# Kernel optimization log

Hardware: AMD Instinct MI355X
Metric: run time of the kernel (lower is better)

## Reference

```python
import jax, jax.numpy as jnp
import numpy as np


def _parallel_scan_affine(log_a, b):
    """Hillis-Steele doubling scan for h_t = a_t*h_{t-1} + b_t (h_0 = 0).

    log_a, b: (B, T, d). Operator: (la2,b2) o (la1,b1) = (la1+la2, exp(la2)*b1 + b2).
    """
    T = log_a.shape[1]
    la, bv = log_a, b
    stride = 1
    while stride < T:  # static Python loop, log2(T) rounds
        la_prev = jnp.roll(la, stride, axis=1).at[:, :stride, :].set(0.0)
        bv_prev = jnp.roll(bv, stride, axis=1).at[:, :stride, :].set(0.0)
        bv = jnp.exp(la) * bv_prev + bv
        la = la + la_prev
        stride *= 2
    return bv


def setup_inputs() -> dict:
    key = jax.random.key(0)
    kx, kwz, kwh = jax.random.split(key, 3)
    B, T, D = 4, 4096, 1024
    x = jax.random.normal(kx, (B, T, D), dtype=jnp.float32)
    # nn.Linear(D, D) weights, stored as (out, in) like torch
    Wz = jax.random.normal(kwz, (D, D), dtype=jnp.float32) * 0.02
    bz = jnp.zeros((D,), dtype=jnp.float32)
    Wh = jax.random.normal(kwh, (D, D), dtype=jnp.float32) * 0.02
    bh = jnp.zeros((D,), dtype=jnp.float32)
    return {"x": x, "Wz": Wz, "bz": bz, "Wh": Wh, "bh": bh}


def reference(x, Wz, bz, Wh, bh):
    # forward_parallel: z = sigmoid(linear_z(x)); h_tilde = linear_h(x)
    z = jax.nn.sigmoid(jnp.einsum("btd,ed->bte", x, Wz) + bz)
    h_tilde = jnp.einsum("btd,ed->bte", x, Wh) + bh
    log_a = jnp.log(1.0 - z + 1e-08)
    b = z * h_tilde
    h_out = _parallel_scan_affine(log_a, b)
    return h_out  # out_proj is Identity since d_inner == d_model
```

## Files before the change

kernel.cpp:

```cpp
#include <hip/hip_runtime.h>
#include <hip/hip_bf16.h>


typedef __bf16 bf16x8 __attribute__((ext_vector_type(8)));
typedef __bf16 bf16x4 __attribute__((ext_vector_type(4)));
typedef float  f32x4  __attribute__((ext_vector_type(4)));

#define BSZ 4
#define TSZ 4096
#define DSZ 1024
#define MSZ (BSZ*TSZ)
#define CH  32
#define NC  (TSZ/CH)

__device__ __forceinline__ void gload_lds16(const __bf16* g, __bf16* l) {
  __builtin_amdgcn_global_load_lds(
      (const __attribute__((address_space(1))) void*)g,
      (__attribute__((address_space(3))) void*)l, 16, 0, 0);
}

__global__ void convert_tile_kernel(const float* __restrict__ X,
                                    const float* __restrict__ Wz,
                                    const float* __restrict__ Wh,
                                    __bf16* __restrict__ Xc,
                                    __bf16* __restrict__ Wzc,
                                    __bf16* __restrict__ Whc)
{
  const int bx = blockIdx.x;
  const float* src; __bf16* dst; int gid;
  if (bx < 8192)      { src = X;  dst = Xc;  gid =  bx        *256 + threadIdx.x; }
  else if (bx < 8704) { src = Wz; dst = Wzc; gid = (bx - 8192)*256 + threadIdx.x; }
  else                { src = Wh; dst = Whc; gid = (bx - 8704)*256 + threadIdx.x; }
  const int l    = gid & 63;
  const int i    = (gid >> 6) & 7;
  const int kblk = (gid >> 9) & 31;
  const int rblk = gid >> 14;
  const int row  = rblk*128 + i*16 + (l & 15);
  const int col  = kblk*32 + (l >> 4)*8;
  const float* g = src + (size_t)row*DSZ + col;
  float4 v0 = *(const float4*)g;
  float4 v1 = *(const float4*)(g + 4);
  bf16x8 p;
  p[0]=(__bf16)v0.x; p[1]=(__bf16)v0.y; p[2]=(__bf16)v0.z; p[3]=(__bf16)v0.w;
  p[4]=(__bf16)v1.x; p[5]=(__bf16)v1.y; p[6]=(__bf16)v1.z; p[7]=(__bf16)v1.w;
  *(bf16x8*)(dst + (size_t)gid*8) = p;
}

__global__ __launch_bounds__(256, 2) void gemm_gate_kernel(
    const __bf16* __restrict__ Xc,  const __bf16* __restrict__ Wzc,
    const __bf16* __restrict__ Whc,
    const float* __restrict__ bz, const float* __restrict__ bh,
    __bf16* __restrict__ a_ws, float* __restrict__ b_out)
{
  __shared__ __align__(16) __bf16 As [4096];
  __shared__ __align__(16) __bf16 Bzs[4096];
  __shared__ __align__(16) __bf16 Bhs[4096];

  const int tid  = threadIdx.x;
  const int lane = tid & 63;
  const int wv   = tid >> 6;
  const int wM   = (wv >> 1) * 64;
  const int wN   = (wv & 1) * 64;
  const int wMg  = wM >> 4;
  const int wNg  = wN >> 4;
  const int lr   = lane & 15;
  const int q    = lane >> 4;
  const int wbase = wv * 64;

  const __bf16* Xb = Xc  + (size_t)blockIdx.x * 32 * 4096;
  const __bf16* Zb = Wzc + (size_t)blockIdx.y * 32 * 4096;
  const __bf16* Hb = Whc + (size_t)blockIdx.y * 32 * 4096;

  f32x4 accz[4][4] = {};
  f32x4 acch[4][4] = {};

  for (int kblk = 0; kblk < 32; ++kblk) {
    __syncthreads();
    const size_t tb = (size_t)kblk * 4096;
    #pragma unroll
    for (int c = 0; c < 2; ++c) {
      const int eo = (c*256 + wbase + lane) * 8;
      const int lo = (c*256 + wbase) * 8;
      gload_lds16(Xb + tb + eo, As  + lo);
      gload_lds16(Zb + tb + eo, Bzs + lo);
      gload_lds16(Hb + tb + eo, Bhs + lo);
    }
    __syncthreads();

    bf16x8 af[4];
    #pragma unroll
    for (int i = 0; i < 4; ++i)
      af[i] = *(const bf16x8*)(As + (wMg + i)*512 + lane*8);
    #pragma unroll
    for (int j = 0; j < 4; ++j) {
      bf16x8 bz8 = *(const bf16x8*)(Bzs + (wNg + j)*512 + lane*8);
      bf16x8 bh8 = *(const bf16x8*)(Bhs + (wNg + j)*512 + lane*8);
      #pragma unroll
      for (int i = 0; i < 4; ++i) {
        accz[j][i] = __builtin_amdgcn_mfma_f32_16x16x32_bf16(af[i], bz8, accz[j][i], 0, 0, 0);
        acch[j][i] = __builtin_amdgcn_mfma_f32_16x16x32_bf16(af[i], bh8, acch[j][i], 0, 0, 0);
      }
    }
  }

  const int M0 = blockIdx.x * 128;
  const int N0 = blockIdx.y * 128;
  #pragma unroll
  for (int j = 0; j < 4; ++j) {
    const int e = N0 + wN + j*16 + lr;
    const float bzv = bz[e];
    const float bhv = bh[e];
    #pragma unroll
    for (int i = 0; i < 4; ++i) {
      const int mbase = M0 + wM + i*16 + q*4;
      #pragma unroll
      for (int r = 0; r < 4; ++r) {
        const size_t idx = (size_t)(mbase + r)*DSZ + e;
        const float pz = accz[j][i][r] + bzv;
        const float ph = acch[j][i][r] + bhv;
        const float ex = __expf(-pz);
        const float z  = 1.0f / (1.0f + ex);
        a_ws[idx]  = (__bf16)fmaf(ex, z, 1e-8f);
        b_out[idx] = z * ph;
      }
    }
  }
}

__global__ void scan_pass1_kernel(const __bf16* __restrict__ a_ws,
                                  const float* __restrict__ b_out,
                                  float* __restrict__ Aprod,
                                  float* __restrict__ Bcomp)
{
  const int bc   = blockIdx.x;
  const int d0   = threadIdx.x * 4;
  const size_t base = (size_t)bc * CH * DSZ + d0;
  float A[4]  = {1.f, 1.f, 1.f, 1.f};
  float Bv[4] = {0.f, 0.f, 0.f, 0.f};
  #pragma unroll 8
  for (int t = 0; t < CH; ++t) {
    bf16x4 a4 = *(const bf16x4*)(a_ws + base + (size_t)t*DSZ);
    float4 b4 = *(const float4*)(b_out + base + (size_t)t*DSZ);
    const float bb[4] = {b4.x, b4.y, b4.z, b4.w};
    #pragma unroll
    for (int c = 0; c < 4; ++c) {
      const float a = (float)a4[c];
      Bv[c] = fmaf(a, Bv[c], bb[c]);
      A[c] *= a;
    }
  }
  const size_t cidx = (size_t)bc*DSZ + d0;
  *(float4*)(Aprod + cidx) = make_float4(A[0], A[1], A[2], A[3]);
  *(float4*)(Bcomp + cidx) = make_float4(Bv[0], Bv[1], Bv[2], Bv[3]);
}

__global__ void scan_pass2_kernel(const float* __restrict__ Aprod,
                                  const float* __restrict__ Bcomp,
                                  float* __restrict__ Hstart)
{
  const int lane = threadIdx.x & 63;
  const int wave = (blockIdx.x * 256 + threadIdx.x) >> 6;
  const int b = wave >> 10;
  const int d = wave & 1023;
  const size_t i0 = (size_t)(b*NC + 2*lane)*DSZ + d;
  const float A0 = Aprod[i0],       B0 = Bcomp[i0];
  const float A1 = Aprod[i0 + DSZ], B1 = Bcomp[i0 + DSZ];
  float A  = A0 * A1;
  float Bv = fmaf(A1, B0, B1);
  #pragma unroll
  for (int s = 1; s < 64; s <<= 1) {
    const float Ap = __shfl_up(A,  s, 64);
    const float Bp = __shfl_up(Bv, s, 64);
    if (lane >= s) { Bv = fmaf(A, Bp, Bv); A *= Ap; }
  }
  float Hp = __shfl_up(Bv, 1, 64);
  if (lane == 0) Hp = 0.0f;
  Hstart[i0]       = Hp;
  Hstart[i0 + DSZ] = fmaf(A0, Hp, B0);
}

__global__ void scan_pass3_kernel(const __bf16* __restrict__ a_ws,
                                  const float* __restrict__ Hstart,
                                  float* __restrict__ out)
{
  const int bc   = blockIdx.x;
  const int d0   = threadIdx.x * 4;
  const size_t base = (size_t)bc * CH * DSZ + d0;
  float4 hv = *(const float4*)(Hstart + (size_t)bc*DSZ + d0);
  float h[4] = {hv.x, hv.y, hv.z, hv.w};
  #pragma unroll 8
  for (int t = 0; t < CH; ++t) {
    bf16x4 a4 = *(const bf16x4*)(a_ws + base + (size_t)t*DSZ);
    float4 b4 = *(const float4*)(out + base + (size_t)t*DSZ);
    const float bb[4] = {b4.x, b4.y, b4.z, b4.w};
    #pragma unroll
    for (int c = 0; c < 4; ++c)
      h[c] = fmaf((float)a4[c], h[c], bb[c]);
    *(float4*)(out + base + (size_t)t*DSZ) = make_float4(h[0], h[1], h[2], h[3]);
  }
}

extern "C" void kernel_launch(void* const* d_in, const int* in_sizes, int n_in,
                              void* d_out, int out_size, void* d_ws, size_t ws_size,
                              hipStream_t stream)
{
  const float* x  = (const float*)d_in[0];
  const float* Wz = (const float*)d_in[1];
  const float* bz = (const float*)d_in[2];
  const float* Wh = (const float*)d_in[3];
  const float* bh = (const float*)d_in[4];
  float* out = (float*)d_out;

  __bf16* Xc   = (__bf16*)d_ws;
  __bf16* Wzc  = Xc  + (size_t)MSZ * DSZ;
  __bf16* Whc  = Wzc + (size_t)DSZ * DSZ;
  __bf16* a_ws = Whc + (size_t)DSZ * DSZ;
  float* Aprod  = (float*)(a_ws + (size_t)MSZ * DSZ);
  float* Bcomp  = Aprod + (size_t)BSZ*NC*DSZ;
  float* Hstart = Bcomp + (size_t)BSZ*NC*DSZ;

  convert_tile_kernel<<<9216, 256, 0, stream>>>(x, Wz, Wh, Xc, Wzc, Whc);
  gemm_gate_kernel<<<dim3(MSZ/128, DSZ/128), 256, 0, stream>>>(Xc, Wzc, Whc, bz, bh, a_ws, out);
  scan_pass1_kernel<<<BSZ*NC, 256, 0, stream>>>(a_ws, out, Aprod, Bcomp);
  scan_pass2_kernel<<<(BSZ*DSZ)/4, 256, 0, stream>>>(Aprod, Bcomp, Hstart);
  scan_pass3_kernel<<<BSZ*NC, 256, 0, stream>>>(a_ws, Hstart, out);
}
```

Baseline: 255.6 us.

## Fuse chunk-local scan reduction into GEMM epilogue, drop scan pass1 kernel

The GEMM epilogue now computes the per-32-row chunk affine composition (A product, B combination) directly from its accumulator values, using in-register sequential combine over 4 rows and cross-quad shuffles, and writes Aprod/Bcomp. This removes the separate scan_pass1 kernel and its full re-read of a_ws and b_out from global memory. In exchange it adds shuffles and register pressure to the GEMM epilogue, and relies on the MFMA output row mapping matching chunk boundaries.

```diff
diff --git a/kernel.cpp b/kernel.cpp
--- a/kernel.cpp
+++ b/kernel.cpp
@@ -50,7 +50,8 @@
     const __bf16* __restrict__ Xc,  const __bf16* __restrict__ Wzc,
     const __bf16* __restrict__ Whc,
     const float* __restrict__ bz, const float* __restrict__ bh,
-    __bf16* __restrict__ a_ws, float* __restrict__ b_out)
+    __bf16* __restrict__ a_ws, float* __restrict__ b_out,
+    float* __restrict__ Aprod, float* __restrict__ Bcomp)
 {
   __shared__ __align__(16) __bf16 As [4096];
   __shared__ __align__(16) __bf16 Bzs[4096];
@@ -110,9 +111,11 @@
     const int e = N0 + wN + j*16 + lr;
     const float bzv = bz[e];
     const float bhv = bh[e];
+    float Aseg[4], Bseg[4];
     #pragma unroll
     for (int i = 0; i < 4; ++i) {
       const int mbase = M0 + wM + i*16 + q*4;
+      float A = 1.0f, Bv = 0.0f;
       #pragma unroll
       for (int r = 0; r < 4; ++r) {
         const size_t idx = (size_t)(mbase + r)*DSZ + e;
@@ -120,38 +123,36 @@
         const float ph = acch[j][i][r] + bhv;
         const float ex = __expf(-pz);
         const float z  = 1.0f / (1.0f + ex);
-        a_ws[idx]  = (__bf16)fmaf(ex, z, 1e-8f);
-        b_out[idx] = z * ph;
-      }
-    }
-  }
-}
-
-__global__ void scan_pass1_kernel(const __bf16* __restrict__ a_ws,
-                                  const float* __restrict__ b_out,
-                                  float* __restrict__ Aprod,
-                                  float* __restrict__ Bcomp)
-{
-  const int bc   = blockIdx.x;
-  const int d0   = threadIdx.x * 4;
-  const size_t base = (size_t)bc * CH * DSZ + d0;
-  float A[4]  = {1.f, 1.f, 1.f, 1.f};
-  float Bv[4] = {0.f, 0.f, 0.f, 0.f};
-  #pragma unroll 8
-  for (int t = 0; t < CH; ++t) {
-    bf16x4 a4 = *(const bf16x4*)(a_ws + base + (size_t)t*DSZ);
-    float4 b4 = *(const float4*)(b_out + base + (size_t)t*DSZ);
-    const float bb[4] = {b4.x, b4.y, b4.z, b4.w};
-    #pragma unroll
-    for (int c = 0; c < 4; ++c) {
-      const float a = (float)a4[c];
-      Bv[c] = fmaf(a, Bv[c], bb[c]);
-      A[c] *= a;
-    }
-  }
-  const size_t cidx = (size_t)bc*DSZ + d0;
-  *(float4*)(Aprod + cidx) = make_float4(A[0], A[1], A[2], A[3]);
-  *(float4*)(Bcomp + cidx) = make_float4(Bv[0], Bv[1], Bv[2], Bv[3]);
+        const __bf16 abf = (__bf16)fmaf(ex, z, 1e-8f);
+        const float  af  = (float)abf;
+        const float  bf  = z * ph;
+        a_ws[idx]  = abf;
+        b_out[idx] = bf;
+        Bv = fmaf(af, Bv, bf);
+        A *= af;
+      }
+      Aseg[i] = A; Bseg[i] = Bv;
+    }
+    #pragma unroll
+    for (int i = 0; i < 4; ++i) {
+      #pragma unroll
+      for (int s = 16; s < 64; s <<= 1) {
+        const float Ap = __shfl_up(Aseg[i], s, 64);
+        const float Bp = __shfl_up(Bseg[i], s, 64);
+        if (lane >= s) { Bseg[i] = fmaf(Aseg[i], Bp, Bseg[i]); Aseg[i] *= Ap; }
+      }
+    }
+    if (q == 3) {
+      #pragma unroll
+      for (int c = 0; c < 2; ++c) {
+        const float Ac = Aseg[2*c+1] * Aseg[2*c];
+        const float Bc = fmaf(Aseg[2*c+1], Bseg[2*c], Bseg[2*c+1]);
+        const int bc = (M0 + wM + c*32) >> 5;
+        Aprod[(size_t)bc*DSZ + e] = Ac;
+        Bcomp[(size_t)bc*DSZ + e] = Bc;
+      }
+    }
+  }
 }
 
 __global__ void scan_pass2_kernel(const float* __restrict__ Aprod,
@@ -220,8 +221,8 @@
   float* Hstart = Bcomp + (size_t)BSZ*NC*DSZ;
 
   convert_tile_kernel<<<9216, 256, 0, stream>>>(x, Wz, Wh, Xc, Wzc, Whc);
-  gemm_gate_kernel<<<dim3(MSZ/128, DSZ/128), 256, 0, stream>>>(Xc, Wzc, Whc, bz, bh, a_ws, out);
-  scan_pass1_kernel<<<BSZ*NC, 256, 0, stream>>>(a_ws, out, Aprod, Bcomp);
+  gemm_gate_kernel<<<dim3(MSZ/128, DSZ/128), 256, 0, stream>>>(
+      Xc, Wzc, Whc, bz, bh, a_ws, out, Aprod, Bcomp);
   scan_pass2_kernel<<<(BSZ*DSZ)/4, 256, 0, stream>>>(Aprod, Bcomp, Hstart);
   scan_pass3_kernel<<<BSZ*NC, 256, 0, stream>>>(a_ws, Hstart, out);
 }
```

New measurement: 244.8 us. -4.2%, faster.
